# Kernel optimization log

Hardware: AMD Instinct MI355X
Metric: run time of the kernel (lower is better)

Reference implementation:

```python
import jax, jax.numpy as jnp
import numpy as np

P = 5.0
A = 10.0
NUM_VARS = 1_000_000
NUM_CLAUSES = 1_000_000
E = 3_000_000  # edges per polarity


def setup_inputs() -> dict:
    key = jax.random.key(0)
    k1, k2, k3, k4, k5 = jax.random.split(key, 5)
    xv = jax.random.uniform(k1, (NUM_VARS, 1), dtype=jnp.float32)
    # clause rows: shuffled arange % NUM_CLAUSES so every clause is non-empty
    cp = jax.random.permutation(k2, jnp.arange(E, dtype=jnp.int64) % NUM_CLAUSES)
    cn = jax.random.permutation(k3, jnp.arange(E, dtype=jnp.int64) % NUM_CLAUSES)
    vp = jax.random.randint(k4, (E,), 0, NUM_VARS, dtype=jnp.int64)
    vn = jax.random.randint(k5, (E,), 0, NUM_VARS, dtype=jnp.int64)
    adj_pos = jnp.stack([cp, vp])  # [2, E]
    adj_neg = jnp.stack([cn, vn])  # [2, E]
    clause_count = jnp.ones((NUM_CLAUSES,), dtype=jnp.float32)
    return {"xv": xv, "adj_pos": adj_pos, "adj_neg": adj_neg, "clause_count": clause_count}


def reference(xv, adj_pos, adj_neg, clause_count):
    x = xv.reshape(-1)            # [V]
    xn = 1.0 - x
    # gather literal values and their exp(p*.) weights along edges
    lit = jnp.concatenate([x[adj_pos[1]], xn[adj_neg[1]]])            # [2E]
    xe = jnp.concatenate([jnp.exp(P * x)[adj_pos[1]], jnp.exp(P * xn)[adj_neg[1]]])  # [2E]
    idx = jnp.concatenate([adj_pos[0], adj_neg[0]])                   # [2E]
    numerator = jax.ops.segment_sum(lit * xe, idx, num_segments=NUM_CLAUSES)
    dominator = jax.ops.segment_sum(xe, idx, num_segments=NUM_CLAUSES)
    # push_to_side: 1/(1+exp(a*(0.5-x))) == sigmoid(a*(x-0.5))
    sm = jax.nn.sigmoid(A * (numerator / dominator - 0.5))            # [NUM_CLAUSES]
    # metric = mse_loss(sm, clause_count)
    loss = jnp.mean((sm - clause_count) ** 2)
    return loss
```

## Files before the change

### kernel.cpp

```cpp
#include <hip/hip_runtime.h>

constexpr int   NUM_CLAUSES = 1000000;
constexpr int   NUM_EDGES   = 3000000;
constexpr float Pc = 5.0f;
constexpr float Ac = 10.0f;

constexpr float FXSCALE = 64.0f;
constexpr float FXINV   = 1.0f / 64.0f;

constexpr int NB  = 250;
constexpr int CPB = 4000;
constexpr int CAP = CPB * 6;

constexpr int TPB   = 512;
constexpr int RPB   = 8192;
constexpr int RPT   = RPB / TPB;
constexpr int NBLKP = (NUM_EDGES + RPB - 1) / RPB;

constexpr float QSCALE = 1048575.0f;
constexpr float QINV   = 1.0f / 1048575.0f;

constexpr size_t OFF_CTR = 24000000;
constexpr size_t OFF_PAR = 24001024;

__device__ __forceinline__ unsigned pack_fx(float num, float den) {
    unsigned lo = (unsigned)(num * FXSCALE + 0.5f);
    unsigned hi = (unsigned)(den * FXSCALE + 0.5f);
    return lo | (hi << 16);
}

__global__ __launch_bounds__(TPB)
void partition_kernel(const int*   __restrict__ adj_pos,
                      const int*   __restrict__ adj_neg,
                      const float* __restrict__ x,
                      unsigned* __restrict__ recs,
                      unsigned* __restrict__ counters) {
    __shared__ unsigned      hist[NB];
    __shared__ unsigned      sbase[NB];
    __shared__ unsigned      lbase[NB];
    __shared__ unsigned      srec[RPB];
    __shared__ unsigned char sbid[RPB];
    __shared__ unsigned      wsum[TPB / 64];
    __shared__ unsigned      woff[TPB / 64];

    const bool neg   = (blockIdx.x >= (unsigned)NBLKP);
    const int  sblk  = neg ? (int)blockIdx.x - NBLKP : (int)blockIdx.x;
    const int  start = sblk * RPB;
    const int  n     = min(RPB, NUM_EDGES - start);
    const int* crow  = neg ? adj_neg : adj_pos;
    const int* vrow  = crow + NUM_EDGES;
    const int  tid   = (int)threadIdx.x;

    for (int b = tid; b < NB; b += TPB) hist[b] = 0;
    __syncthreads();

    int cc_[RPT], vv_[RPT];
    if (n == RPB) {
        #pragma unroll
        for (int j = 0; j < RPT / 4; ++j) {
            int4 c4 = ((const int4*)(crow + start))[j * TPB + tid];
            int4 v4 = ((const int4*)(vrow + start))[j * TPB + tid];
            cc_[4*j] = c4.x; cc_[4*j+1] = c4.y; cc_[4*j+2] = c4.z; cc_[4*j+3] = c4.w;
            vv_[4*j] = v4.x; vv_[4*j+1] = v4.y; vv_[4*j+2] = v4.z; vv_[4*j+3] = v4.w;
        }
    } else {
        #pragma unroll
        for (int r = 0; r < RPT; ++r) {
            int pos = 4 * ((r >> 2) * TPB + tid) + (r & 3);
            cc_[r] = (pos < n) ? crow[start + pos] : -1;
            vv_[r] = (pos < n) ? vrow[start + pos] : 0;
        }
    }

    float xv[RPT];
    #pragma unroll
    for (int r = 0; r < RPT; ++r) xv[r] = x[vv_[r]];

    unsigned rec[RPT], meta[RPT];
    #pragma unroll
    for (int r = 0; r < RPT; ++r) {
        meta[r] = 0xFFFFFFFFu;
        if (cc_[r] >= 0) {
            int   c   = cc_[r];
            int   b   = c / CPB;
            float lit = neg ? (1.0f - xv[r]) : xv[r];
            unsigned q = (unsigned)(lit * QSCALE + 0.5f);
            rec[r] = (q << 12) | (unsigned)(c - b * CPB);
            unsigned rank = atomicAdd(&hist[b], 1u);
            meta[r] = ((unsigned)b << 13) | rank;
        }
    }
    __syncthreads();

    unsigned h    = (tid < NB) ? hist[tid] : 0u;
    unsigned incl = h;
    #pragma unroll
    for (int off = 1; off < 64; off <<= 1) {
        unsigned t = __shfl_up(incl, off, 64);
        if ((tid & 63) >= off) incl += t;
    }
    if ((tid & 63) == 63) wsum[tid >> 6] = incl;
    __syncthreads();
    if (tid == 0) {
        unsigned a = 0;
        #pragma unroll
        for (int w = 0; w < TPB / 64; ++w) { woff[w] = a; a += wsum[w]; }
    }
    __syncthreads();
    if (tid < NB) {
        lbase[tid] = incl - h + woff[tid >> 6];
        sbase[tid] = h ? atomicAdd(&counters[tid], h) : 0u;
    }
    __syncthreads();

    #pragma unroll
    for (int r = 0; r < RPT; ++r) {
        if (meta[r] != 0xFFFFFFFFu) {
            unsigned b    = meta[r] >> 13;
            unsigned rank = meta[r] & 0x1FFFu;
            unsigned p    = lbase[b] + rank;
            srec[p] = rec[r];
            sbid[p] = (unsigned char)b;
        }
    }
    __syncthreads();

    for (int p = tid; p < n; p += TPB) {
        unsigned b = sbid[p];
        recs[(size_t)b * CAP + sbase[b] + ((unsigned)p - lbase[b])] = srec[p];
    }
}

__global__ __launch_bounds__(1024)
void bucket_loss_kernel(const uint4* __restrict__ recs4,
                        const float* __restrict__ cc,
                        float* __restrict__ partials) {
    __shared__ unsigned lacc[CPB];
    const int b = blockIdx.x;
    for (int j = threadIdx.x; j < CPB; j += 1024) lacc[j] = 0;
    __syncthreads();

    const uint4* r4 = recs4 + (size_t)b * (CAP / 4);
    for (int k = threadIdx.x; k < CAP / 4; k += 1024) {
        uint4 e = r4[k];
        #pragma unroll
        for (int k2 = 0; k2 < 4; ++k2) {
            unsigned r  = (&e.x)[k2];
            float lit = (float)(r >> 12) * QINV;
            float w   = __expf(Pc * lit);
            atomicAdd(&lacc[r & 0xFFFu], pack_fx(lit * w, w));
        }
    }
    __syncthreads();

    float v = 0.0f;
    const float* gc = cc + (size_t)b * CPB;
    for (int j = threadIdx.x; j < CPB; j += 1024) {
        unsigned a   = lacc[j];
        float    num = (float)(a & 0xffffu) * FXINV;
        float    den = (float)(a >> 16)     * FXINV;
        float    sm  = 1.0f / (1.0f + __expf(-Ac * (num / den - 0.5f)));
        float    e0  = sm - gc[j];
        v += e0 * e0;
    }
    v *= 1.0f / (float)NUM_CLAUSES;

    #pragma unroll
    for (int off = 32; off > 0; off >>= 1)
        v += __shfl_down(v, off, 64);

    __shared__ float partial[16];
    int lane = threadIdx.x & 63;
    int wid  = threadIdx.x >> 6;
    if (lane == 0) partial[wid] = v;
    __syncthreads();
    if (threadIdx.x == 0) {
        float s = 0.f;
        #pragma unroll
        for (int w = 0; w < 16; ++w) s += partial[w];
        partials[b] = s;
    }
}

__global__ void final_kernel(const float* __restrict__ partials,
                             float* __restrict__ out, int n) {
    float v = 0.0f;
    for (int i = threadIdx.x; i < n; i += 256) v += partials[i];

    #pragma unroll
    for (int off = 32; off > 0; off >>= 1)
        v += __shfl_down(v, off, 64);

    __shared__ float partial[4];
    int lane = threadIdx.x & 63;
    int wid  = threadIdx.x >> 6;
    if (lane == 0) partial[wid] = v;
    __syncthreads();
    if (threadIdx.x == 0)
        out[0] = partial[0] + partial[1] + partial[2] + partial[3];
}

extern "C" void kernel_launch(void* const* d_in, const int* in_sizes, int n_in,
                              void* d_out, int out_size, void* d_ws, size_t ws_size,
                              hipStream_t stream) {
    const float* xv      = (const float*)d_in[0];
    const int*   adj_pos = (const int*)  d_in[1];
    const int*   adj_neg = (const int*)  d_in[2];
    const float* cc      = (const float*)d_in[3];

    char* ws = (char*)d_ws;
    unsigned* recs     = (unsigned*)ws;
    unsigned* counters = (unsigned*)(ws + OFF_CTR);
    float*    partials = (float*)   (ws + OFF_PAR);
    float*    out      = (float*)d_out;

    hipMemsetAsync(counters, 0, NB * sizeof(unsigned), stream);

    partition_kernel<<<2 * NBLKP, TPB, 0, stream>>>(adj_pos, adj_neg, xv,
                                                    recs, counters);

    bucket_loss_kernel<<<NB, 1024, 0, stream>>>((const uint4*)recs, cc, partials);

    final_kernel<<<1, 256, 0, stream>>>(partials, out, NB);
}
```

Before: 144.8 us.

## Double bucket count, pad global counters, rotate counter atomics, defer record packing

Splits clauses into 500 buckets of 2000 instead of 250 of 4000 and doubles the partition block size to 1024 threads. Global bucket counters are padded to separate cache lines, and each block walks the buckets starting at a block-dependent offset, so atomics on the same counter are spread out in time. Record packing is moved after the histogram scan and overlaps the global counter atomics, with the bucket id widened to 16 bits and the local index shrunk to 11 bits. The aim is less global atomic contention and more bucket-kernel blocks, at the cost of more, smaller scatter segments and a larger counter memset. The quantized literal keeps 20 bits, and its top bit still fits because the shift dropped from 12 to 11.

```diff
diff --git a/kernel.cpp b/kernel.cpp
--- a/kernel.cpp
+++ b/kernel.cpp
@@ -8,11 +8,11 @@
 constexpr float FXSCALE = 64.0f;
 constexpr float FXINV   = 1.0f / 64.0f;
 
-constexpr int NB  = 250;
-constexpr int CPB = 4000;
+constexpr int NB  = 500;
+constexpr int CPB = 2000;
 constexpr int CAP = CPB * 6;
 
-constexpr int TPB   = 512;
+constexpr int TPB   = 1024;
 constexpr int RPB   = 8192;
 constexpr int RPT   = RPB / TPB;
 constexpr int NBLKP = (NUM_EDGES + RPB - 1) / RPB;
@@ -20,8 +20,10 @@
 constexpr float QSCALE = 1048575.0f;
 constexpr float QINV   = 1.0f / 1048575.0f;
 
+constexpr int CSTRIDE = 16;
+
 constexpr size_t OFF_CTR = 24000000;
-constexpr size_t OFF_PAR = 24001024;
+constexpr size_t OFF_PAR = OFF_CTR + (size_t)NB * CSTRIDE * 4;
 
 __device__ __forceinline__ unsigned pack_fx(float num, float den) {
     unsigned lo = (unsigned)(num * FXSCALE + 0.5f);
@@ -29,19 +31,19 @@
     return lo | (hi << 16);
 }
 
-__global__ __launch_bounds__(TPB)
+__global__ __launch_bounds__(TPB, 8)
 void partition_kernel(const int*   __restrict__ adj_pos,
                       const int*   __restrict__ adj_neg,
                       const float* __restrict__ x,
                       unsigned* __restrict__ recs,
                       unsigned* __restrict__ counters) {
-    __shared__ unsigned      hist[NB];
-    __shared__ unsigned      sbase[NB];
-    __shared__ unsigned      lbase[NB];
-    __shared__ unsigned      srec[RPB];
-    __shared__ unsigned char sbid[RPB];
-    __shared__ unsigned      wsum[TPB / 64];
-    __shared__ unsigned      woff[TPB / 64];
+    __shared__ unsigned       hist[NB];
+    __shared__ unsigned       sbase[NB];
+    __shared__ unsigned       lbase[NB];
+    __shared__ unsigned       srec[RPB];
+    __shared__ unsigned short sbid[RPB];
+    __shared__ unsigned       wsum[TPB / 64];
+    __shared__ unsigned       woff[TPB / 64];
 
     const bool neg   = (blockIdx.x >= (unsigned)NBLKP);
     const int  sblk  = neg ? (int)blockIdx.x - NBLKP : (int)blockIdx.x;
@@ -51,7 +53,7 @@
     const int* vrow  = crow + NUM_EDGES;
     const int  tid   = (int)threadIdx.x;
 
-    for (int b = tid; b < NB; b += TPB) hist[b] = 0;
+    if (tid < NB) hist[tid] = 0;
     __syncthreads();
 
     int cc_[RPT], vv_[RPT];
@@ -76,16 +78,12 @@
     #pragma unroll
     for (int r = 0; r < RPT; ++r) xv[r] = x[vv_[r]];
 
-    unsigned rec[RPT], meta[RPT];
+    unsigned meta[RPT];
     #pragma unroll
     for (int r = 0; r < RPT; ++r) {
         meta[r] = 0xFFFFFFFFu;
         if (cc_[r] >= 0) {
-            int   c   = cc_[r];
-            int   b   = c / CPB;
-            float lit = neg ? (1.0f - xv[r]) : xv[r];
-            unsigned q = (unsigned)(lit * QSCALE + 0.5f);
-            rec[r] = (q << 12) | (unsigned)(c - b * CPB);
+            int b = cc_[r] / CPB;
             unsigned rank = atomicAdd(&hist[b], 1u);
             meta[r] = ((unsigned)b << 13) | rank;
         }
@@ -107,22 +105,33 @@
         for (int w = 0; w < TPB / 64; ++w) { woff[w] = a; a += wsum[w]; }
     }
     __syncthreads();
+    if (tid < NB) lbase[tid] = incl - h + woff[tid >> 6];
+    __syncthreads();
+
+    unsigned myres = 0;
+    int      rb    = 0;
     if (tid < NB) {
-        lbase[tid] = incl - h + woff[tid >> 6];
-        sbase[tid] = h ? atomicAdd(&counters[tid], h) : 0u;
-    }
-    __syncthreads();
+        int boff = (int)blockIdx.x;
+        if (boff >= NB) boff -= NB;
+        rb = tid + boff;
+        if (rb >= NB) rb -= NB;
+        myres = atomicAdd(&counters[rb * CSTRIDE], hist[rb]);
+    }
 
     #pragma unroll
     for (int r = 0; r < RPT; ++r) {
-        if (meta[r] != 0xFFFFFFFFu) {
+        if (cc_[r] >= 0) {
             unsigned b    = meta[r] >> 13;
             unsigned rank = meta[r] & 0x1FFFu;
+            int      loc  = cc_[r] - (int)b * CPB;
+            float    lit  = neg ? (1.0f - xv[r]) : xv[r];
+            unsigned q    = (unsigned)(lit * QSCALE + 0.5f);
             unsigned p    = lbase[b] + rank;
-            srec[p] = rec[r];
-            sbid[p] = (unsigned char)b;
-        }
-    }
+            srec[p] = (q << 11) | (unsigned)loc;
+            sbid[p] = (unsigned short)b;
+        }
+    }
+    if (tid < NB) sbase[rb] = myres;
     __syncthreads();
 
     for (int p = tid; p < n; p += TPB) {
@@ -131,7 +140,7 @@
     }
 }
 
-__global__ __launch_bounds__(1024)
+__global__ __launch_bounds__(1024, 8)
 void bucket_loss_kernel(const uint4* __restrict__ recs4,
                         const float* __restrict__ cc,
                         float* __restrict__ partials) {
@@ -146,9 +155,9 @@
         #pragma unroll
         for (int k2 = 0; k2 < 4; ++k2) {
             unsigned r  = (&e.x)[k2];
-            float lit = (float)(r >> 12) * QINV;
+            float lit = (float)(r >> 11) * QINV;
             float w   = __expf(Pc * lit);
-            atomicAdd(&lacc[r & 0xFFFu], pack_fx(lit * w, w));
+            atomicAdd(&lacc[r & 0x7FFu], pack_fx(lit * w, w));
         }
     }
     __syncthreads();
@@ -214,7 +223,7 @@
     float*    partials = (float*)   (ws + OFF_PAR);
     float*    out      = (float*)d_out;
 
-    hipMemsetAsync(counters, 0, NB * sizeof(unsigned), stream);
+    hipMemsetAsync(counters, 0, (size_t)NB * CSTRIDE * sizeof(unsigned), stream);
 
     partition_kernel<<<2 * NBLKP, TPB, 0, stream>>>(adj_pos, adj_neg, xv,
                                                     recs, counters);
```

After: 143.9 us. No clear change (-0.6%).

## Replace bucket partition with direct global packed atomics per clause

Applied to the files above, without the earlier changes.

Drops the two-pass scheme that binned edge records into clause buckets through shared memory and then reduced them with LDS atomics. Each edge now computes its exp weight in the scatter kernel and does one global atomicAdd of a packed fixed-point (num, den) word into a per-clause accumulator array, which the loss kernel then reads. This removes the record write/read traffic and the scan and sync overhead, at the cost of 6M random global atomics and a 4MB memset. Block size changes to 256 threads and buckets to 500×2000.

```diff
diff --git a/kernel.cpp b/kernel.cpp
--- a/kernel.cpp
+++ b/kernel.cpp
@@ -8,20 +8,18 @@
 constexpr float FXSCALE = 64.0f;
 constexpr float FXINV   = 1.0f / 64.0f;
 
-constexpr int NB  = 250;
-constexpr int CPB = 4000;
-constexpr int CAP = CPB * 6;
-
-constexpr int TPB   = 512;
-constexpr int RPB   = 8192;
-constexpr int RPT   = RPB / TPB;
-constexpr int NBLKP = (NUM_EDGES + RPB - 1) / RPB;
-
 constexpr float QSCALE = 1048575.0f;
 constexpr float QINV   = 1.0f / 1048575.0f;
 
-constexpr size_t OFF_CTR = 24000000;
-constexpr size_t OFF_PAR = 24001024;
+constexpr int TPB   = 256;
+constexpr int RPT   = 16;
+constexpr int RPB   = TPB * RPT;
+constexpr int NBLKP = (NUM_EDGES + RPB - 1) / RPB;
+
+constexpr int NB  = 500;
+constexpr int CPB = 2000;
+
+constexpr size_t OFF_PAR = 4000000;
 
 __device__ __forceinline__ unsigned pack_fx(float num, float den) {
     unsigned lo = (unsigned)(num * FXSCALE + 0.5f);
@@ -30,19 +28,10 @@
 }
 
 __global__ __launch_bounds__(TPB)
-void partition_kernel(const int*   __restrict__ adj_pos,
-                      const int*   __restrict__ adj_neg,
-                      const float* __restrict__ x,
-                      unsigned* __restrict__ recs,
-                      unsigned* __restrict__ counters) {
-    __shared__ unsigned      hist[NB];
-    __shared__ unsigned      sbase[NB];
-    __shared__ unsigned      lbase[NB];
-    __shared__ unsigned      srec[RPB];
-    __shared__ unsigned char sbid[RPB];
-    __shared__ unsigned      wsum[TPB / 64];
-    __shared__ unsigned      woff[TPB / 64];
-
+void scatter_kernel(const int*   __restrict__ adj_pos,
+                    const int*   __restrict__ adj_neg,
+                    const float* __restrict__ x,
+                    unsigned* __restrict__ acc) {
     const bool neg   = (blockIdx.x >= (unsigned)NBLKP);
     const int  sblk  = neg ? (int)blockIdx.x - NBLKP : (int)blockIdx.x;
     const int  start = sblk * RPB;
@@ -51,16 +40,16 @@
     const int* vrow  = crow + NUM_EDGES;
     const int  tid   = (int)threadIdx.x;
 
-    for (int b = tid; b < NB; b += TPB) hist[b] = 0;
-    __syncthreads();
-
     int cc_[RPT], vv_[RPT];
     if (n == RPB) {
         #pragma unroll
         for (int j = 0; j < RPT / 4; ++j) {
             int4 c4 = ((const int4*)(crow + start))[j * TPB + tid];
+            cc_[4*j] = c4.x; cc_[4*j+1] = c4.y; cc_[4*j+2] = c4.z; cc_[4*j+3] = c4.w;
+        }
+        #pragma unroll
+        for (int j = 0; j < RPT / 4; ++j) {
             int4 v4 = ((const int4*)(vrow + start))[j * TPB + tid];
-            cc_[4*j] = c4.x; cc_[4*j+1] = c4.y; cc_[4*j+2] = c4.z; cc_[4*j+3] = c4.w;
             vv_[4*j] = v4.x; vv_[4*j+1] = v4.y; vv_[4*j+2] = v4.z; vv_[4*j+3] = v4.w;
         }
     } else {
@@ -76,87 +65,30 @@
     #pragma unroll
     for (int r = 0; r < RPT; ++r) xv[r] = x[vv_[r]];
 
-    unsigned rec[RPT], meta[RPT];
     #pragma unroll
     for (int r = 0; r < RPT; ++r) {
-        meta[r] = 0xFFFFFFFFu;
         if (cc_[r] >= 0) {
-            int   c   = cc_[r];
-            int   b   = c / CPB;
-            float lit = neg ? (1.0f - xv[r]) : xv[r];
-            unsigned q = (unsigned)(lit * QSCALE + 0.5f);
-            rec[r] = (q << 12) | (unsigned)(c - b * CPB);
-            unsigned rank = atomicAdd(&hist[b], 1u);
-            meta[r] = ((unsigned)b << 13) | rank;
+            float    lit = neg ? (1.0f - xv[r]) : xv[r];
+            unsigned q   = (unsigned)(lit * QSCALE + 0.5f);
+            float    lq  = (float)q * QINV;
+            float    w   = __expf(Pc * lq);
+            atomicAdd(&acc[cc_[r]], pack_fx(lq * w, w));
         }
-    }
-    __syncthreads();
-
-    unsigned h    = (tid < NB) ? hist[tid] : 0u;
-    unsigned incl = h;
-    #pragma unroll
-    for (int off = 1; off < 64; off <<= 1) {
-        unsigned t = __shfl_up(incl, off, 64);
-        if ((tid & 63) >= off) incl += t;
-    }
-    if ((tid & 63) == 63) wsum[tid >> 6] = incl;
-    __syncthreads();
-    if (tid == 0) {
-        unsigned a = 0;
-        #pragma unroll
-        for (int w = 0; w < TPB / 64; ++w) { woff[w] = a; a += wsum[w]; }
-    }
-    __syncthreads();
-    if (tid < NB) {
-        lbase[tid] = incl - h + woff[tid >> 6];
-        sbase[tid] = h ? atomicAdd(&counters[tid], h) : 0u;
-    }
-    __syncthreads();
-
-    #pragma unroll
-    for (int r = 0; r < RPT; ++r) {
-        if (meta[r] != 0xFFFFFFFFu) {
-            unsigned b    = meta[r] >> 13;
-            unsigned rank = meta[r] & 0x1FFFu;
-            unsigned p    = lbase[b] + rank;
-            srec[p] = rec[r];
-            sbid[p] = (unsigned char)b;
-        }
-    }
-    __syncthreads();
-
-    for (int p = tid; p < n; p += TPB) {
-        unsigned b = sbid[p];
-        recs[(size_t)b * CAP + sbase[b] + ((unsigned)p - lbase[b])] = srec[p];
     }
 }
 
 __global__ __launch_bounds__(1024)
-void bucket_loss_kernel(const uint4* __restrict__ recs4,
-                        const float* __restrict__ cc,
-                        float* __restrict__ partials) {
-    __shared__ unsigned lacc[CPB];
-    const int b = blockIdx.x;
-    for (int j = threadIdx.x; j < CPB; j += 1024) lacc[j] = 0;
-    __syncthreads();
-
-    const uint4* r4 = recs4 + (size_t)b * (CAP / 4);
-    for (int k = threadIdx.x; k < CAP / 4; k += 1024) {
-        uint4 e = r4[k];
-        #pragma unroll
-        for (int k2 = 0; k2 < 4; ++k2) {
-            unsigned r  = (&e.x)[k2];
-            float lit = (float)(r >> 12) * QINV;
-            float w   = __expf(Pc * lit);
-            atomicAdd(&lacc[r & 0xFFFu], pack_fx(lit * w, w));
-        }
-    }
-    __syncthreads();
+void loss_kernel(const unsigned* __restrict__ acc,
+                 const float* __restrict__ cc,
+                 float* __restrict__ partials) {
+    const int b   = blockIdx.x;
+    const int tid = (int)threadIdx.x;
 
     float v = 0.0f;
-    const float* gc = cc + (size_t)b * CPB;
-    for (int j = threadIdx.x; j < CPB; j += 1024) {
-        unsigned a   = lacc[j];
+    const unsigned* ga = acc + (size_t)b * CPB;
+    const float*    gc = cc  + (size_t)b * CPB;
+    for (int j = tid; j < CPB; j += 1024) {
+        unsigned a   = ga[j];
         float    num = (float)(a & 0xffffu) * FXINV;
         float    den = (float)(a >> 16)     * FXINV;
         float    sm  = 1.0f / (1.0f + __expf(-Ac * (num / den - 0.5f)));
@@ -170,11 +102,11 @@
         v += __shfl_down(v, off, 64);
 
     __shared__ float partial[16];
-    int lane = threadIdx.x & 63;
-    int wid  = threadIdx.x >> 6;
+    int lane = tid & 63;
+    int wid  = tid >> 6;
     if (lane == 0) partial[wid] = v;
     __syncthreads();
-    if (threadIdx.x == 0) {
+    if (tid == 0) {
         float s = 0.f;
         #pragma unroll
         for (int w = 0; w < 16; ++w) s += partial[w];
@@ -209,17 +141,15 @@
     const float* cc      = (const float*)d_in[3];
 
     char* ws = (char*)d_ws;
-    unsigned* recs     = (unsigned*)ws;
-    unsigned* counters = (unsigned*)(ws + OFF_CTR);
-    float*    partials = (float*)   (ws + OFF_PAR);
+    unsigned* acc      = (unsigned*)ws;
+    float*    partials = (float*)(ws + OFF_PAR);
     float*    out      = (float*)d_out;
 
-    hipMemsetAsync(counters, 0, NB * sizeof(unsigned), stream);
+    hipMemsetAsync(acc, 0, (size_t)NUM_CLAUSES * sizeof(unsigned), stream);
 
-    partition_kernel<<<2 * NBLKP, TPB, 0, stream>>>(adj_pos, adj_neg, xv,
-                                                    recs, counters);
+    scatter_kernel<<<2 * NBLKP, TPB, 0, stream>>>(adj_pos, adj_neg, xv, acc);
 
-    bucket_loss_kernel<<<NB, 1024, 0, stream>>>((const uint4*)recs, cc, partials);
+    loss_kernel<<<NB, 1024, 0, stream>>>(acc, cc, partials);
 
     final_kernel<<<1, 256, 0, stream>>>(partials, out, NB);
 }
```

Measured after the change: 325.7 us. +124.9%, slower.
